# Kernel tuning notes

Hardware: AMD Instinct MI355X
Metric: run time of the kernel (lower is better)

The kernel has to match this reference:

```python
import jax, jax.numpy as jnp
import numpy as np

B, T, DM = 4, 2048, 1024
H, DK, DV = 16, 64, 64


def setup_inputs() -> dict:
    key = jax.random.key(0)
    k1, k2, k3, k4 = jax.random.split(key, 4)
    x = jax.random.normal(k1, (B, T, DM), dtype=jnp.float32)
    scale = 0.02
    Wq = jax.random.normal(k2, (H, DM, DK), dtype=jnp.float32) * scale
    Wk = jax.random.normal(k3, (H, DM, DK), dtype=jnp.float32) * scale
    Wv = jax.random.normal(k4, (H, DM, DV), dtype=jnp.float32) * scale
    return {"x": x, "Wq": Wq, "Wk": Wk, "Wv": Wv}


def reference(x, Wq, Wk, Wv):
    # Per-head projections, vectorized over heads: [B,H,T,dk]
    q = jnp.einsum('btd,hdk->bhtk', x, Wq)
    k = jnp.einsum('btd,hdk->bhtk', x, Wk)
    v = jnp.einsum('btd,hdv->bhtv', x, Wv)
    scale = DK ** -0.5  # k.shape[-1] ** -0.5 in original
    wei = jnp.einsum('bhtk,bhsk->bhts', q, k) * scale  # [B,H,T,T]
    causal = jnp.tril(jnp.ones((T, T), dtype=bool))
    wei = jnp.where(causal, wei, -jnp.inf)
    wei = jax.nn.softmax(wei, axis=-1)
    # dropout p=0.0 -> identity (eval-mode equivalent)
    out = jnp.einsum('bhts,bhsv->bhtv', wei, v)  # [B,H,T,dv]
    # concat heads along last dim: [B,T,H*dv]
    return out.transpose(0, 2, 1, 3).reshape(B, T, H * DV)
```

## Files before the change

### kernel.cpp

```cpp
#include <hip/hip_runtime.h>


#define B_  4
#define T_  2048
#define DM_ 1024
#define H_  16
#define D_  64
#define DMO 1024

typedef unsigned short u16;
typedef unsigned int   u32;
typedef u16   u16x8  __attribute__((ext_vector_type(8)));
typedef short s16x8  __attribute__((ext_vector_type(8)));
typedef float f32x4  __attribute__((ext_vector_type(4)));
typedef float f32x16 __attribute__((ext_vector_type(16)));
typedef u32   u32x2  __attribute__((ext_vector_type(2)));
typedef u32   u32x4  __attribute__((ext_vector_type(4)));

#if __has_builtin(__builtin_amdgcn_exp2f)
#define EXP2(x) __builtin_amdgcn_exp2f(x)
#else
#define EXP2(x) __expf((x) * 0.69314718f)
#endif

__device__ __forceinline__ u16 f2bf_hu(float f) {
    u32 u = __builtin_bit_cast(u32, f) + 0x8000u;
    return (u16)(u >> 16);
}
__device__ __forceinline__ u32 pk2(float lo, float hi) {
    u32 ul = __builtin_bit_cast(u32, lo) + 0x8000u;
    u32 uh = __builtin_bit_cast(u32, hi) + 0x8000u;
    return __builtin_amdgcn_perm(uh, ul, 0x07060302);
}
__device__ __forceinline__ u16x8 cvt8(const float* s) {
    f32x4 a = *(const f32x4*)s;
    f32x4 b = *(const f32x4*)(s + 4);
    u32x4 r { pk2(a[0], a[1]), pk2(a[2], a[3]), pk2(b[0], b[1]), pk2(b[2], b[3]) };
    return __builtin_bit_cast(u16x8, r);
}
__device__ __forceinline__ f32x4 mfma16(u16x8 a, u16x8 b, f32x4 c) {
    return __builtin_amdgcn_mfma_f32_16x16x32_bf16(
        __builtin_bit_cast(s16x8, a), __builtin_bit_cast(s16x8, b), c, 0, 0, 0);
}
__device__ __forceinline__ f32x16 mfma32(u16x8 a, u16x8 b, f32x16 c) {
    return __builtin_amdgcn_mfma_f32_32x32x16_bf16(
        __builtin_bit_cast(s16x8, a), __builtin_bit_cast(s16x8, b), c, 0, 0, 0);
}
__device__ __forceinline__ void gld_lds16(const u16* g, u16* l) {
    __builtin_amdgcn_global_load_lds(
        (const __attribute__((address_space(1))) u32*)g,
        (__attribute__((address_space(3))) u32*)l, 16, 0, 0);
}

__global__ __launch_bounds__(256) void cvt_x(const float* __restrict__ x,
                                             u16* __restrict__ xb) {
    size_t i0 = ((size_t)blockIdx.x * 256 + threadIdx.x) * 32;
    #pragma unroll
    for (int c = 0; c < 4; c++)
        *(u16x8*)(xb + i0 + c * 8) = cvt8(x + i0 + c * 8);
}

__global__ __launch_bounds__(256) void cvt_w(
    const float* __restrict__ Wq, const float* __restrict__ Wk,
    const float* __restrict__ Wv, u16* __restrict__ Wt) {
    __shared__ u16 L[64][74];
    const int dblk = blockIdx.x, h = blockIdx.y, mat = blockIdx.z;
    const float* W = (mat == 0) ? Wq : (mat == 1) ? Wk : Wv;
    const int tid = threadIdx.x;
    {
        const int dl = tid >> 2, c = (tid & 3) * 16;
        const float* src = W + ((size_t)h * DM_ + dblk * 64 + dl) * D_ + c;
        #pragma unroll
        for (int g = 0; g < 2; g++)
            *(u16x8*)&L[dl][c + g * 8] = cvt8(src + g * 8);
    }
    __syncthreads();
    {
        const int dkr = tid >> 2, g = tid & 3;
        u16 tmp[16];
        #pragma unroll
        for (int j = 0; j < 16; j++) tmp[j] = L[g * 16 + j][dkr];
        u16* dst = Wt + ((size_t)(mat * 16 + h) * 64 + dkr) * DM_ + dblk * 64 + g * 16;
        *(u16x8*)dst = *(u16x8*)tmp;
        *(u16x8*)(dst + 8) = *(u16x8*)(tmp + 8);
    }
}

template<int SWAP>
__device__ __forceinline__ void pcompute(const char* Asb, const char* Bsb,
                                         int wm, int wn, int quad, int l16,
                                         int ax, f32x4 (&acc)[4][4]) {
    #pragma unroll
    for (int ks = 0; ks < 2; ks++) {
        u16x8 af[4], bf[4];
        #pragma unroll
        for (int i = 0; i < 4; i++)
            af[i] = *(const u16x8*)(Asb +
                ((((wm * 64 + i * 16 + l16) * 64 + ks * 32 + quad * 8) * 2) ^ ax));
        #pragma unroll
        for (int j = 0; j < 4; j++)
            bf[j] = *(const u16x8*)(Bsb +
                ((((wn * 64 + j * 16 + l16) * 64 + ks * 32 + quad * 8) * 2) ^ ax));
        #pragma unroll
        for (int i = 0; i < 4; i++)
            #pragma unroll
            for (int j = 0; j < 4; j++)
                acc[i][j] = SWAP ? mfma16(bf[j], af[i], acc[i][j])
                                 : mfma16(af[i], bf[j], acc[i][j]);
    }
}

__global__ __launch_bounds__(256) void proj_kernel(
    const u16* __restrict__ xb, const u16* __restrict__ Wt,
    u16* __restrict__ Qc, u16* __restrict__ Kc, u16* __restrict__ Vtc)
{
    __shared__ __attribute__((aligned(16))) u16 As0[128][64];
    __shared__ __attribute__((aligned(16))) u16 Bs0[128][64];
    __shared__ __attribute__((aligned(16))) u16 As1[128][64];
    __shared__ __attribute__((aligned(16))) u16 Bs1[128][64];

    const int pb = blockIdx.x;
    const int wg = (pb & 7) * 192 + (pb >> 3);
    const int m0 = (wg & 63) * 128;
    const int n0 = (wg >> 6) * 128;
    const int mat = n0 >> 10;
    const int tid  = threadIdx.x;
    const int wave = tid >> 6, lane = tid & 63;
    const int quad = lane >> 4, l16 = lane & 15;
    const int wm   = wave >> 1, wn = wave & 1;

    const int r8 = lane >> 3, g8 = lane & 7;
    const int gs = (g8 ^ r8) * 8;
    const int ax = (l16 & 7) << 4;

    f32x4 acc[4][4];
    #pragma unroll
    for (int i = 0; i < 4; i++)
        #pragma unroll
        for (int j = 0; j < 4; j++) acc[i][j] = f32x4{0.f, 0.f, 0.f, 0.f};

    auto STAGE = [&](u16* Ad, u16* Bd, int kb) {
        const int kbase = kb * 64;
        #pragma unroll
        for (int it = 0; it < 4; it++) {
            const int row = it * 32 + wave * 8 + r8;
            const int ldo = (it * 4 + wave) * 512 + lane * 8;
            gld_lds16(xb + (size_t)(m0 + row) * DM_ + kbase + gs, Ad + ldo);
            gld_lds16(Wt + (size_t)(n0 + row) * DM_ + kbase + gs, Bd + ldo);
        }
    };

    STAGE(&As0[0][0], &Bs0[0][0], 0);
    __syncthreads();

    #define PLOOP(SW)                                                        \
        for (int kb = 0; kb < 16; kb += 2) {                                 \
            STAGE(&As1[0][0], &Bs1[0][0], kb + 1);                           \
            pcompute<SW>((const char*)As0, (const char*)Bs0,                 \
                         wm, wn, quad, l16, ax, acc);                        \
            __syncthreads();                                                 \
            if (kb + 2 < 16) STAGE(&As0[0][0], &Bs0[0][0], kb + 2);          \
            pcompute<SW>((const char*)As1, (const char*)Bs1,                 \
                         wm, wn, quad, l16, ax, acc);                        \
            __syncthreads();                                                 \
        }
    if (mat != 2) { PLOOP(1) } else { PLOOP(0) }
    #undef PLOOP

    const int h_base = (n0 & 1023) >> 6;
    if (mat != 2) {
        u16* Cm = (mat == 0) ? Qc : Kc;
        const float sc = (mat == 0) ? 0.18033688f : 1.0f;
        #pragma unroll
        for (int i = 0; i < 4; i++) {
            const int m  = m0 + wm * 64 + i * 16 + l16;
            const int bb = m >> 11, t = m & (T_ - 1);
            u16* rowp = Cm + ((size_t)(bb * H_ + h_base + wn) * T_ + t) * D_;
            #pragma unroll
            for (int j = 0; j < 4; j++) {
                const int dk0 = j * 16 + quad * 4;
                u32x2 d { pk2(acc[i][j][0] * sc, acc[i][j][1] * sc),
                          pk2(acc[i][j][2] * sc, acc[i][j][3] * sc) };
                *(u32x2*)(rowp + dk0) = d;
            }
        }
    } else {
        #pragma unroll
        for (int i = 0; i < 4; i++) {
            const int m  = m0 + wm * 64 + i * 16 + quad * 4;
            const int bb = m >> 11, t = m & (T_ - 1);
            #pragma unroll
            for (int j = 0; j < 4; j++) {
                const int dk = j * 16 + l16;
                u32x2 d { pk2(acc[i][j][0], acc[i][j][1]),
                          pk2(acc[i][j][2], acc[i][j][3]) };
                *(u32x2*)(Vtc + ((size_t)(bb * H_ + h_base + wn) * D_ + dk) * T_ + t) = d;
            }
        }
    }
}

__global__ __launch_bounds__(128, 3) void attn_kernel(
    const u16* __restrict__ Qc, const u16* __restrict__ Kc,
    const u16* __restrict__ Vtc, float* __restrict__ out)
{
    __shared__ __attribute__((aligned(16))) u16 Ks[64][64];
    __shared__ __attribute__((aligned(16))) u16 Vs[64][64];

    const int pb = blockIdx.x;
    const int lb = (pb & 7) * 256 + (pb >> 3);
    const int qt = 31 - (lb & 31);
    const int h  = (lb >> 5) & 15, b = lb >> 9;

    const int tid = threadIdx.x, w = tid >> 6, lane = tid & 63;
    const int l31 = lane & 31, hi = lane >> 5;
    const int r8 = lane >> 3, g8 = lane & 7;
    const int gs = (g8 ^ r8) * 8;
    const int ax = (l31 & 7) << 4;

    const u16* Qbh = Qc + (size_t)(b * H_ + h) * T_ * D_;
    const u16* Kbh = Kc + (size_t)(b * H_ + h) * T_ * D_;
    const u16* Vbh = Vtc + (size_t)(b * H_ + h) * D_ * T_;
    u16* Ksp = &Ks[0][0];
    u16* Vsp = &Vs[0][0];
    const char* Ksb = (const char*)Ksp;
    const char* Vsb = (const char*)Vsp;

    const int q0 = qt * 64;
    const int qrow = q0 + w * 32 + l31;
    const int qloc = w * 32 + l31;

    u16x8 qf[4];
    #pragma unroll
    for (int ks = 0; ks < 4; ks++)
        qf[ks] = *(const u16x8*)(Qbh + (size_t)qrow * D_ + ks * 16 + hi * 8);

    f32x16 ot0, ot1;
    #pragma unroll
    for (int r = 0; r < 16; r++) { ot0[r] = 0.f; ot1[r] = 0.f; }
    float mi = -1e30f, li = 0.f;

    const int nst = qt + 1;
    for (int st = 0; st < nst; st++) {
        const int sbase = st * 64;
        __syncthreads();
        #pragma unroll
        for (int i = 0; i < 4; i++) {
            const int seg = i * 2 + w;
            const int row = seg * 8 + r8;
            const int ldo = seg * 512 + lane * 8;
            gld_lds16(Kbh + (size_t)(sbase + row) * D_ + gs, Ksp + ldo);
            gld_lds16(Vbh + (size_t)row * T_ + sbase + gs,  Vsp + ldo);
        }
        __syncthreads();

        f32x16 st0, st1;
        #pragma unroll
        for (int r = 0; r < 16; r++) { st0[r] = 0.f; st1[r] = 0.f; }
        #pragma unroll
        for (int ks = 0; ks < 4; ks++) {
            const int co = (ks * 16 + hi * 8) * 2;
            u16x8 k0 = *(const u16x8*)(Ksb + ((l31 * 128 + co) ^ ax));
            u16x8 k1 = *(const u16x8*)(Ksb + (((32 + l31) * 128 + co) ^ ax));
            st0 = mfma32(k0, qf[ks], st0);
            st1 = mfma32(k1, qf[ks], st1);
        }

        if (st == nst - 1) {
            #pragma unroll
            for (int r = 0; r < 16; r++) {
                const int sl = (r & 3) + 8 * (r >> 2) + 4 * hi;
                if (sl > qloc)      st0[r] = -1e30f;
                if (sl + 32 > qloc) st1[r] = -1e30f;
            }
        }

        float mx = -1e30f;
        #pragma unroll
        for (int r = 0; r < 16; r++) mx = fmaxf(mx, fmaxf(st0[r], st1[r]));
        mx = fmaxf(mx, __shfl_xor(mx, 32));
        if (!__all(mx - mi <= 8.f)) {
            const float mn = fmaxf(mi, mx);
            const float al = EXP2(mi - mn);
            li *= al;
            #pragma unroll
            for (int r = 0; r < 16; r++) { ot0[r] *= al; ot1[r] *= al; }
            mi = mn;
        }
        float sum = 0.f;
        #pragma unroll
        for (int r = 0; r < 16; r++) {
            const float p0 = EXP2(st0[r] - mi);
            const float p1 = EXP2(st1[r] - mi);
            st0[r] = p0; st1[r] = p1;
            sum += p0 + p1;
        }
        sum += __shfl_xor(sum, 32);
        li += sum;

        u16x8 pb4[4];
        #define PACK(SRC, C, OUT) {                                           \
            u32 d0 = pk2(SRC[8*(C)+0], SRC[8*(C)+1]);                         \
            u32 d1 = pk2(SRC[8*(C)+2], SRC[8*(C)+3]);                         \
            u32 d2 = pk2(SRC[8*(C)+4], SRC[8*(C)+5]);                         \
            u32 d3 = pk2(SRC[8*(C)+6], SRC[8*(C)+7]);                         \
            u32 e0 = __shfl_xor(hi ? d0 : d2, 32);                            \
            u32 e1 = __shfl_xor(hi ? d1 : d3, 32);                            \
            u32x4 wds{ hi ? e0 : d0, hi ? e1 : d1,                            \
                       hi ? d2 : e0, hi ? d3 : e1 };                          \
            OUT = __builtin_bit_cast(u16x8, wds); }
        PACK(st0, 0, pb4[0]); PACK(st0, 1, pb4[1]);
        PACK(st1, 0, pb4[2]); PACK(st1, 1, pb4[3]);
        #undef PACK

        #pragma unroll
        for (int kc = 0; kc < 4; kc++) {
            const int co = (kc * 16 + hi * 8) * 2;
            u16x8 v0 = *(const u16x8*)(Vsb + ((l31 * 128 + co) ^ ax));
            u16x8 v1 = *(const u16x8*)(Vsb + (((32 + l31) * 128 + co) ^ ax));
            ot0 = mfma32(v0, pb4[kc], ot0);
            ot1 = mfma32(v1, pb4[kc], ot1);
        }
    }

    const float inv = 1.0f / li;
    float* orow = out + (size_t)(b * T_ + qrow) * DMO + h * D_;
    #pragma unroll
    for (int c = 0; c < 2; c++)
        #pragma unroll
        for (int hf = 0; hf < 2; hf++) {
            f32x4 v0, v1;
            #pragma unroll
            for (int j = 0; j < 4; j++) {
                v0[j] = ot0[c * 8 + hf * 4 + j] * inv;
                v1[j] = ot1[c * 8 + hf * 4 + j] * inv;
            }
            *(f32x4*)(orow + c * 16 + hf * 8 + hi * 4)      = v0;
            *(f32x4*)(orow + 32 + c * 16 + hf * 8 + hi * 4) = v1;
        }
}

extern "C" void kernel_launch(void* const* d_in, const int* in_sizes, int n_in,
                              void* d_out, int out_size, void* d_ws, size_t ws_size,
                              hipStream_t stream) {
    int xi = 0, wi[3] = {1, 2, 3};
    {
        int k = 0, found = 0;
        for (int i = 0; i < n_in && i < 8; i++) {
            if (in_sizes[i] == B_ * T_ * DM_) { xi = i; found = 1; }
            else if (in_sizes[i] == H_ * DM_ * D_ && k < 3) wi[k++] = i;
        }
        if (!found || k != 3) { xi = 0; wi[0] = 1; wi[1] = 2; wi[2] = 3; }
    }
    const float* x  = (const float*)d_in[xi];
    const float* Wq = (const float*)d_in[wi[0]];
    const float* Wk = (const float*)d_in[wi[1]];
    const float* Wv = (const float*)d_in[wi[2]];
    float* out = (float*)d_out;

    u16* xb = (u16*)d_out;
    u16* Wt = xb + (size_t)B_ * T_ * DM_;
    const size_t per = (size_t)B_ * H_ * T_ * D_;
    u16* Qc  = (u16*)d_ws;
    u16* Kc  = Qc + per;
    u16* Vtc = Kc + per;

    cvt_x<<<1024, 256, 0, stream>>>(x, xb);
    cvt_w<<<dim3(16, 16, 3), 256, 0, stream>>>(Wq, Wk, Wv, Wt);
    proj_kernel<<<1536, 256, 0, stream>>>(xb, Wt, Qc, Kc, Vtc);
    attn_kernel<<<2048, 128, 0, stream>>>(Qc, Kc, Vtc, out);
}
```

Measured before the change: 251.4 us.

## Pair causal query tiles per block, double-buffer K/V loads, merge convert kernels

```diff
diff --git a/kernel.cpp b/kernel.cpp
--- a/kernel.cpp
+++ b/kernel.cpp
@@ -52,19 +52,22 @@
         (__attribute__((address_space(3))) u32*)l, 16, 0, 0);
 }
 
-__global__ __launch_bounds__(256) void cvt_x(const float* __restrict__ x,
-                                             u16* __restrict__ xb) {
-    size_t i0 = ((size_t)blockIdx.x * 256 + threadIdx.x) * 32;
-    #pragma unroll
-    for (int c = 0; c < 4; c++)
-        *(u16x8*)(xb + i0 + c * 8) = cvt8(x + i0 + c * 8);
-}
-
-__global__ __launch_bounds__(256) void cvt_w(
-    const float* __restrict__ Wq, const float* __restrict__ Wk,
-    const float* __restrict__ Wv, u16* __restrict__ Wt) {
+__global__ __launch_bounds__(256) void cvt_all(
+    const float* __restrict__ x,  const float* __restrict__ Wq,
+    const float* __restrict__ Wk, const float* __restrict__ Wv,
+    u16* __restrict__ xb, u16* __restrict__ Wt)
+{
     __shared__ u16 L[64][74];
-    const int dblk = blockIdx.x, h = blockIdx.y, mat = blockIdx.z;
+    const int bx = blockIdx.x;
+    if (bx < 1024) {
+        size_t i0 = ((size_t)bx * 256 + threadIdx.x) * 32;
+        #pragma unroll
+        for (int c = 0; c < 4; c++)
+            *(u16x8*)(xb + i0 + c * 8) = cvt8(x + i0 + c * 8);
+        return;
+    }
+    const int wb = bx - 1024;
+    const int dblk = wb & 15, h = (wb >> 4) & 15, mat = wb >> 8;
     const float* W = (mat == 0) ? Wq : (mat == 1) ? Wk : Wv;
     const int tid = threadIdx.x;
     {
@@ -200,36 +203,46 @@
     }
 }
 
-__global__ __launch_bounds__(128, 3) void attn_kernel(
+__global__ __launch_bounds__(128, 2) void attn_kernel(
     const u16* __restrict__ Qc, const u16* __restrict__ Kc,
     const u16* __restrict__ Vtc, float* __restrict__ out)
 {
-    __shared__ __attribute__((aligned(16))) u16 Ks[64][64];
-    __shared__ __attribute__((aligned(16))) u16 Vs[64][64];
+    __shared__ __attribute__((aligned(16))) u16 Ks[2][64][64];
+    __shared__ __attribute__((aligned(16))) u16 Vs[2][64][64];
 
     const int pb = blockIdx.x;
-    const int lb = (pb & 7) * 256 + (pb >> 3);
-    const int qt = 31 - (lb & 31);
-    const int h  = (lb >> 5) & 15, b = lb >> 9;
+    const int lb = (pb & 7) * 128 + (pb >> 3);
+    const int pr = lb & 15;
+    const int bh = lb >> 4;
+    const int h  = bh & 15, b = bh >> 4;
+    const int qa = pr, qb = 31 - pr;
 
     const int tid = threadIdx.x, w = tid >> 6, lane = tid & 63;
     const int l31 = lane & 31, hi = lane >> 5;
     const int r8 = lane >> 3, g8 = lane & 7;
     const int gs = (g8 ^ r8) * 8;
     const int ax = (l31 & 7) << 4;
+    const int qloc = w * 32 + l31;
 
     const u16* Qbh = Qc + (size_t)(b * H_ + h) * T_ * D_;
     const u16* Kbh = Kc + (size_t)(b * H_ + h) * T_ * D_;
     const u16* Vbh = Vtc + (size_t)(b * H_ + h) * D_ * T_;
-    u16* Ksp = &Ks[0][0];
-    u16* Vsp = &Vs[0][0];
-    const char* Ksb = (const char*)Ksp;
-    const char* Vsb = (const char*)Vsp;
-
-    const int q0 = qt * 64;
-    const int qrow = q0 + w * 32 + l31;
-    const int qloc = w * 32 + l31;
-
+
+    auto STAGE = [&](int buf, int t) {
+        const int sbase = t * 64;
+        u16* Kd = &Ks[buf][0][0];
+        u16* Vd = &Vs[buf][0][0];
+        #pragma unroll
+        for (int i2 = 0; i2 < 4; i2++) {
+            const int seg = i2 * 2 + w;
+            const int row = seg * 8 + r8;
+            const int ldo = seg * 512 + lane * 8;
+            gld_lds16(Kbh + (size_t)(sbase + row) * D_ + gs, Kd + ldo);
+            gld_lds16(Vbh + (size_t)row * T_ + sbase + gs,  Vd + ldo);
+        }
+    };
+
+    int qrow = qa * 64 + qloc;
     u16x8 qf[4];
     #pragma unroll
     for (int ks = 0; ks < 4; ks++)
@@ -240,23 +253,41 @@
     for (int r = 0; r < 16; r++) { ot0[r] = 0.f; ot1[r] = 0.f; }
     float mi = -1e30f, li = 0.f;
 
-    const int nst = qt + 1;
-    for (int st = 0; st < nst; st++) {
-        const int sbase = st * 64;
-        __syncthreads();
-        #pragma unroll
-        for (int i = 0; i < 4; i++) {
-            const int seg = i * 2 + w;
-            const int row = seg * 8 + r8;
-            const int ldo = seg * 512 + lane * 8;
-            gld_lds16(Kbh + (size_t)(sbase + row) * D_ + gs, Ksp + ldo);
-            gld_lds16(Vbh + (size_t)row * T_ + sbase + gs,  Vsp + ldo);
-        }
-        __syncthreads();
+    auto EPI = [&]() {
+        const float inv = 1.0f / li;
+        float* orow = out + (size_t)(b * T_ + qrow) * DMO + h * D_;
+        #pragma unroll
+        for (int c = 0; c < 2; c++)
+            #pragma unroll
+            for (int hf = 0; hf < 2; hf++) {
+                f32x4 v0, v1;
+                #pragma unroll
+                for (int j = 0; j < 4; j++) {
+                    v0[j] = ot0[c * 8 + hf * 4 + j] * inv;
+                    v1[j] = ot1[c * 8 + hf * 4 + j] * inv;
+                }
+                *(f32x4*)(orow + c * 16 + hf * 8 + hi * 4)      = v0;
+                *(f32x4*)(orow + 32 + c * 16 + hf * 8 + hi * 4) = v1;
+            }
+    };
+
+    STAGE(0, 0);
+    __syncthreads();
+    int cur = 0;
+
+    for (int i = 0; i <= 32; i++) {
+        if (i < 32) {
+            const int nx = i + 1;
+            const int tn = (nx <= qa) ? nx : nx - qa - 1;
+            STAGE(cur ^ 1, tn);
+        }
+        const char* Ksb = (const char*)&Ks[cur][0][0];
+        const char* Vsb = (const char*)&Vs[cur][0][0];
 
         f32x16 st0, st1;
         #pragma unroll
         for (int r = 0; r < 16; r++) { st0[r] = 0.f; st1[r] = 0.f; }
+        __builtin_amdgcn_s_setprio(1);
         #pragma unroll
         for (int ks = 0; ks < 4; ks++) {
             const int co = (ks * 16 + hi * 8) * 2;
@@ -265,8 +296,9 @@
             st0 = mfma32(k0, qf[ks], st0);
             st1 = mfma32(k1, qf[ks], st1);
         }
-
-        if (st == nst - 1) {
+        __builtin_amdgcn_s_setprio(0);
+
+        if (i == qa || i == 32) {
             #pragma unroll
             for (int r = 0; r < 16; r++) {
                 const int sl = (r & 3) + 8 * (r >> 2) + 4 * hi;
@@ -313,6 +345,7 @@
         PACK(st1, 0, pb4[2]); PACK(st1, 1, pb4[3]);
         #undef PACK
 
+        __builtin_amdgcn_s_setprio(1);
         #pragma unroll
         for (int kc = 0; kc < 4; kc++) {
             const int co = (kc * 16 + hi * 8) * 2;
@@ -321,23 +354,22 @@
             ot0 = mfma32(v0, pb4[kc], ot0);
             ot1 = mfma32(v1, pb4[kc], ot1);
         }
-    }
-
-    const float inv = 1.0f / li;
-    float* orow = out + (size_t)(b * T_ + qrow) * DMO + h * D_;
-    #pragma unroll
-    for (int c = 0; c < 2; c++)
-        #pragma unroll
-        for (int hf = 0; hf < 2; hf++) {
-            f32x4 v0, v1;
-            #pragma unroll
-            for (int j = 0; j < 4; j++) {
-                v0[j] = ot0[c * 8 + hf * 4 + j] * inv;
-                v1[j] = ot1[c * 8 + hf * 4 + j] * inv;
-            }
-            *(f32x4*)(orow + c * 16 + hf * 8 + hi * 4)      = v0;
-            *(f32x4*)(orow + 32 + c * 16 + hf * 8 + hi * 4) = v1;
-        }
+        __builtin_amdgcn_s_setprio(0);
+
+        if (i == qa) {
+            EPI();
+            qrow = qb * 64 + qloc;
+            #pragma unroll
+            for (int ks = 0; ks < 4; ks++)
+                qf[ks] = *(const u16x8*)(Qbh + (size_t)qrow * D_ + ks * 16 + hi * 8);
+            #pragma unroll
+            for (int r = 0; r < 16; r++) { ot0[r] = 0.f; ot1[r] = 0.f; }
+            mi = -1e30f; li = 0.f;
+        }
+        __syncthreads();
+        cur ^= 1;
+    }
+    EPI();
 }
 
 extern "C" void kernel_launch(void* const* d_in, const int* in_sizes, int n_in,
@@ -365,8 +397,7 @@
     u16* Kc  = Qc + per;
     u16* Vtc = Kc + per;
 
-    cvt_x<<<1024, 256, 0, stream>>>(x, xb);
-    cvt_w<<<dim3(16, 16, 3), 256, 0, stream>>>(Wq, Wk, Wv, Wt);
+    cvt_all<<<1792, 256, 0, stream>>>(x, Wq, Wk, Wv, xb, Wt);
     proj_kernel<<<1536, 256, 0, stream>>>(xb, Wt, Qc, Kc, Vtc);
-    attn_kernel<<<2048, 128, 0, stream>>>(Qc, Kc, Vtc, out);
-}
+    attn_kernel<<<1024, 128, 0, stream>>>(Qc, Kc, Vtc, out);
+}
```

Result: faster. 240.2 us (-4.4%).
